# Performance work log

Measured on AMD Instinct MI355X. Metric: run time of the kernel, lower is better.

Reference implementation:

```python
import jax, jax.numpy as jnp
import numpy as np

N = 51200      # total nodes
G = 256        # graphs in batch
NPG = 200      # nodes per graph
E = 409600     # intra-graph edges
EPG = E // G
F_IN, HID, HEADS, NCLS = 768, 128, 4, 2


def setup_inputs() -> dict:
    key = jax.random.key(0)
    ks = jax.random.split(key, 20)
    x = jax.random.normal(ks[0], (N, F_IN), jnp.float32)
    # edges strictly inside each graph, no self-loops (PyG batching semantics)
    gid = jnp.arange(E, dtype=jnp.int32) // EPG
    sl = jax.random.randint(ks[1], (E,), 0, NPG, dtype=jnp.int32)
    off = jax.random.randint(ks[2], (E,), 1, NPG, dtype=jnp.int32)
    dl = (sl + off) % NPG
    edge_index = jnp.stack([gid * NPG + sl, gid * NPG + dl])
    batch = jnp.arange(N, dtype=jnp.int32) // NPG

    def glorot(k, shape, fan_in):
        return jax.random.normal(k, shape, jnp.float32) * np.float32(1.0 / np.sqrt(fan_in))

    return {
        'x': x, 'edge_index': edge_index, 'batch': batch,
        'W1': glorot(ks[3], (F_IN, HEADS * HID), F_IN),
        'a_src1': glorot(ks[4], (HEADS, HID), HID),
        'a_dst1': glorot(ks[5], (HEADS, HID), HID),
        'b1': jnp.zeros((HEADS * HID,), jnp.float32),
        'W2': glorot(ks[6], (HEADS * HID, HID), HEADS * HID),
        'a_src2': glorot(ks[7], (1, HID), HID),
        'a_dst2': glorot(ks[8], (1, HID), HID),
        'b2': jnp.zeros((HID,), jnp.float32),
        'Wc': glorot(ks[9], (HID, 2), HID),
        'bc': jnp.zeros((2,), jnp.float32),
        'Wf1': glorot(ks[10], (HID, HID), HID),
        'bf1': jnp.zeros((HID,), jnp.float32),
        'Wf2': glorot(ks[11], (HID, NCLS), HID),
        'bf2': jnp.zeros((NCLS,), jnp.float32),
    }


def _segment_softmax(logits, seg, num):
    m = jax.ops.segment_max(logits, seg, num_segments=num)
    e = jnp.exp(logits - m[seg])
    s = jax.ops.segment_sum(e, seg, num_segments=num)
    return e / (s[seg] + 1e-16)


def _gat(x, src, dst, W, a_s, a_d, b, n):
    # PyG GATConv, eval mode (attention dropout off), self-loops already in src/dst
    H, C = a_s.shape
    h = (x @ W).reshape(n, H, C)                       # [n,H,C]
    a_src = (h * a_s).sum(-1)                          # [n,H]
    a_dst = (h * a_d).sum(-1)
    logits = jax.nn.leaky_relu(a_src[src] + a_dst[dst], 0.2)  # [Etot,H]
    alpha = _segment_softmax(logits, dst, n)
    out = jax.ops.segment_sum(h[src] * alpha[:, :, None], dst, num_segments=n)
    return out.reshape(n, H * C) + b


def reference(x, edge_index, batch, W1, a_src1, a_dst1, b1, W2, a_src2, a_dst2, b2,
              Wc, bc, Wf1, bf1, Wf2, bf2):
    src0, dst0 = edge_index[0], edge_index[1]
    loop = jnp.arange(N, dtype=src0.dtype)
    src = jnp.concatenate([src0, loop])
    dst = jnp.concatenate([dst0, loop])

    h1 = jax.nn.relu(_gat(x, src, dst, W1, a_src1, a_dst1, b1, N))     # [N,512]
    h2 = jax.nn.relu(_gat(h1, src, dst, W2, a_src2, a_dst2, b2, N))    # [N,128]

    S = jax.nn.softmax(h2 @ Wc + bc, axis=1)                           # [N,2]

    # aggregate(): per-graph S^T A S via per-edge outer products (A from original edges)
    eg = batch[src0]
    outer = S[src0][:, :, None] * S[dst0][:, None, :]                  # [E,2,2]
    agg = jax.ops.segment_sum(outer, eg, num_segments=G)               # [G,2,2]
    rnorm = jnp.clip(jnp.abs(agg).sum(axis=2, keepdims=True), 1e-5, None)  # F.normalize p=1 dim=1
    nadj = agg / rnorm
    diag = jnp.diagonal(nadj, axis1=1, axis2=2)                        # [G,2]
    aggregate_loss = jnp.mean(jnp.mean((diag - 1.0) ** 2, axis=1))     # MSE vs ones, averaged over graphs

    # subgraph embedding: first row of S_g^T x_g per graph
    sub = jax.ops.segment_sum(S[:, 0:1] * h2, batch, num_segments=G)   # [G,128]

    out = jax.nn.relu(sub @ Wf1 + bf1)                                 # eval: dropout off
    out = out @ Wf2 + bf2                                              # [G,2]
    return out, aggregate_loss
```

## Files before the change

kernel.cpp:

```cpp
#include <hip/hip_runtime.h>
#include <hip/hip_bf16.h>
#include <cstdint>

#define N_NODES 51200
#define N_GRAPH 256
#define NPG     200
#define N_EDGE  409600
#define EPG     1600
#define F_IN    768
#define HID     128
#define HEADS   4
#define HC      512

typedef __attribute__((ext_vector_type(8))) short short8;
typedef __attribute__((ext_vector_type(4))) float floatx4;

constexpr size_t OFF_H1B    = 0;
constexpr size_t OFF_H2B    = OFF_H1B + (size_t)N_NODES * HC * 2;
constexpr size_t OFF_H2F    = OFF_H2B + (size_t)N_NODES * HID * 2;
constexpr size_t OFF_WT1    = OFF_H2F + (size_t)N_NODES * HID * 4;
constexpr size_t OFF_WT2    = OFF_WT1 + (size_t)HC * F_IN * 2;
constexpr size_t OFF_S      = OFF_WT2 + (size_t)HID * HC * 2;
constexpr size_t OFF_AGG    = OFF_S + (size_t)N_NODES * 2 * 4;
constexpr size_t OFF_SUB    = OFF_AGG + (size_t)N_GRAPH * 4 * 4;

__device__ __forceinline__ float leaky(float x) { return x >= 0.0f ? x : 0.2f * x; }

__device__ __forceinline__ unsigned short f2bf(float f) {
    unsigned int u = __float_as_uint(f);
    u += 0x7fffu + ((u >> 16) & 1u);
    return (unsigned short)(u >> 16);
}
__device__ __forceinline__ float bflo(int p) { return __uint_as_float((unsigned)p << 16); }
__device__ __forceinline__ float bfhi(int p) { return __uint_as_float((unsigned)p & 0xffff0000u); }

__device__ __forceinline__ void gl_lds16(const void* g, void* l) {
    __builtin_amdgcn_global_load_lds(
        (__attribute__((address_space(1))) void*)(g),
        (__attribute__((address_space(3))) void*)(l),
        16, 0, 0);
}

__global__ __launch_bounds__(256)
void transpose_cvt_kernel(const float* __restrict__ W, short* __restrict__ Wt,
                          int K, int Nn)
{
    int idx = blockIdx.x * 256 + threadIdx.x;
    if (idx >= K * Nn) return;
    int k = idx / Nn, n = idx % Nn;
    Wt[(size_t)n * K + k] = (short)f2bf(W[idx]);
}

template <bool A_BF16>
__global__ __launch_bounds__(256)
void gemm_mfma_kernel(const void* __restrict__ Av, const short* __restrict__ Bt,
                      unsigned short* __restrict__ C, int M, int Nn, int K)
{
    __shared__ __align__(16) short Ablob[4096];
    __shared__ __align__(16) short Bblob[4096];
    const int tid = threadIdx.x;
    const int w = tid >> 6, l = tid & 63;
    const int m0 = blockIdx.x * 128, n0 = blockIdx.y * 128;
    const int wr = w >> 1, wc = w & 1;

    floatx4 acc[4][4];
#pragma unroll
    for (int i = 0; i < 4; ++i)
#pragma unroll
        for (int j = 0; j < 4; ++j) acc[i][j] = (floatx4)0.0f;

    const short* bgp = Bt + (size_t)(n0 + (w * 2) * 16 + (l & 15)) * K + ((l >> 4) * 8);

    const float* Af = (const float*)Av;
    const short* Ab = (const short*)Av;
    const int r = tid >> 1, hh = tid & 1;
    const float* arow = Af + (size_t)(m0 + r) * K + hh * 16;
    const short* agp = Ab + (size_t)(m0 + (w * 2) * 16 + (l & 15)) * K + ((l >> 4) * 8);

    float4 pf0, pf1, pf2, pf3;
    if constexpr (!A_BF16) {
        pf0 = *(const float4*)(arow + 0);
        pf1 = *(const float4*)(arow + 4);
        pf2 = *(const float4*)(arow + 8);
        pf3 = *(const float4*)(arow + 12);
    }

    for (int k0 = 0; k0 < K; k0 += 32) {
        __syncthreads();
        if constexpr (A_BF16) {
            gl_lds16(agp + k0,          &Ablob[(w * 2) * 512]);
            gl_lds16(agp + 16 * K + k0, &Ablob[(w * 2 + 1) * 512]);
        } else {
            unsigned short us[16];
            us[0]=f2bf(pf0.x); us[1]=f2bf(pf0.y); us[2]=f2bf(pf0.z); us[3]=f2bf(pf0.w);
            us[4]=f2bf(pf1.x); us[5]=f2bf(pf1.y); us[6]=f2bf(pf1.z); us[7]=f2bf(pf1.w);
            us[8]=f2bf(pf2.x); us[9]=f2bf(pf2.y); us[10]=f2bf(pf2.z); us[11]=f2bf(pf2.w);
            us[12]=f2bf(pf3.x); us[13]=f2bf(pf3.y); us[14]=f2bf(pf3.z); us[15]=f2bf(pf3.w);
            const int o = (r >> 4) * 512 + (2 * hh) * 128 + (r & 15) * 8;
            short8 v0, v1;
#pragma unroll
            for (int j = 0; j < 8; ++j) { v0[j] = (short)us[j]; v1[j] = (short)us[8 + j]; }
            *(short8*)&Ablob[o]       = v0;
            *(short8*)&Ablob[o + 128] = v1;
        }
        gl_lds16(bgp + k0,          &Bblob[(w * 2) * 512]);
        gl_lds16(bgp + 16 * K + k0, &Bblob[(w * 2 + 1) * 512]);
        __syncthreads();

        if constexpr (!A_BF16) {
            if (k0 + 32 < K) {
                pf0 = *(const float4*)(arow + k0 + 32);
                pf1 = *(const float4*)(arow + k0 + 36);
                pf2 = *(const float4*)(arow + k0 + 40);
                pf3 = *(const float4*)(arow + k0 + 44);
            }
        }

        short8 af[4], bfr[4];
#pragma unroll
        for (int mi = 0; mi < 4; ++mi)
            af[mi] = *(const short8*)&Ablob[(wr * 4 + mi) * 512 + l * 8];
#pragma unroll
        for (int ni = 0; ni < 4; ++ni)
            bfr[ni] = *(const short8*)&Bblob[(wc * 4 + ni) * 512 + l * 8];
#pragma unroll
        for (int mi = 0; mi < 4; ++mi)
#pragma unroll
            for (int ni = 0; ni < 4; ++ni)
                acc[mi][ni] = __builtin_amdgcn_mfma_f32_16x16x32_bf16(
                    af[mi], bfr[ni], acc[mi][ni], 0, 0, 0);
    }

    const int lr = (l >> 4) * 4, lc = l & 15;
#pragma unroll
    for (int mi = 0; mi < 4; ++mi)
#pragma unroll
        for (int ni = 0; ni < 4; ++ni) {
            const size_t base = (size_t)(m0 + wr * 64 + mi * 16 + lr) * Nn
                              + (n0 + wc * 64 + ni * 16 + lc);
#pragma unroll
            for (int rr = 0; rr < 4; ++rr)
                C[base + (size_t)rr * Nn] = f2bf(acc[mi][ni][rr]);
        }
}

__global__ __launch_bounds__(512)
void gat1_kernel(const unsigned short* __restrict__ H, const int* __restrict__ src0,
                 const int* __restrict__ dst0, const float* __restrict__ a_s,
                 const float* __restrict__ a_d, const float* __restrict__ b1,
                 unsigned short* __restrict__ out)
{
    const int g = blockIdx.x, h = blockIdx.y;
    __shared__ int   s_feat[NPG * 64];
    __shared__ float s_as[NPG], s_ad[NPG], s_m[NPG], s_inv[NPG];
    __shared__ int   s_row[NPG + 1];
    __shared__ int   s_cnt[NPG];
    __shared__ int   s_scan[256];
    __shared__ unsigned short s_eraw[EPG];
    __shared__ int2  s_wc[EPG];
    const int tid = threadIdx.x, w = tid >> 6, l = tid & 63;
    const int gbase = g * NPG;

    for (int flat = tid; flat < NPG * 16; flat += 512) {
        int row = flat >> 4, q = flat & 15;
        uint4 v = *(const uint4*)(H + (size_t)(gbase + row) * HC + h * HID + q * 8);
        *(uint4*)&s_feat[row * 64 + q * 4] = v;
    }
    for (int j = tid; j < EPG; j += 512) {
        int s = src0[g * EPG + j] - gbase;
        int d = dst0[g * EPG + j] - gbase;
        s_eraw[j] = (unsigned short)(s | (d << 8));
    }
    if (tid < NPG) s_cnt[tid] = 0;
    __syncthreads();

    for (int j = tid; j < EPG; j += 512)
        atomicAdd(&s_cnt[s_eraw[j] >> 8], 1);
    const float2 av = ((const float2*)(a_s + h * HID))[l];
    const float2 dv = ((const float2*)(a_d + h * HID))[l];
    for (int nl = w; nl < NPG; nl += 8) {
        int pk = s_feat[nl * 64 + l];
        float f0 = bflo(pk), f1 = bfhi(pk);
        float ss = f0 * av.x + f1 * av.y;
        float sd = f0 * dv.x + f1 * dv.y;
#pragma unroll
        for (int off = 1; off < 64; off <<= 1) {
            ss += __shfl_xor(ss, off);
            sd += __shfl_xor(sd, off);
        }
        if (l == 0) { s_as[nl] = ss; s_ad[nl] = sd; }
    }
    __syncthreads();

    {
        int v = (tid < NPG) ? s_cnt[tid] : 0;
        if (tid < 256) s_scan[tid] = v;
        __syncthreads();
        for (int off = 1; off < 256; off <<= 1) {
            int u = (tid >= off && tid < 256) ? s_scan[tid - off] : 0;
            __syncthreads();
            if (tid < 256) s_scan[tid] += u;
            __syncthreads();
        }
        if (tid < NPG) s_row[tid + 1] = s_scan[tid];
        if (tid == 0) s_row[0] = 0;
        __syncthreads();
        if (tid < NPG) s_scan[tid] = s_row[tid];
    }
    __syncthreads();

    for (int j = tid; j < EPG; j += 512) {
        int pk = s_eraw[j];
        int p = atomicAdd(&s_scan[pk >> 8], 1);
        s_wc[p].y = pk;
    }
    __syncthreads();

    for (int j = tid; j < EPG; j += 512) {
        int pk = s_wc[j].y;
        s_wc[j].x = __float_as_int(leaky(s_as[pk & 255] + s_ad[pk >> 8]));
    }
    __syncthreads();

    if (tid < NPG) {
        float m = leaky(s_as[tid] + s_ad[tid]);
        int r0 = s_row[tid], r1 = s_row[tid + 1];
        for (int j = r0; j < r1; ++j) m = fmaxf(m, __int_as_float(s_wc[j].x));
        s_m[tid] = m;
    }
    __syncthreads();

    for (int j = tid; j < EPG; j += 512) {
        int2 e = s_wc[j];
        s_wc[j].x = __float_as_int(__expf(__int_as_float(e.x) - s_m[e.y >> 8]));
    }
    __syncthreads();

    if (tid < NPG) {
        float rs = __expf(leaky(s_as[tid] + s_ad[tid]) - s_m[tid]);
        int r0 = s_row[tid], r1 = s_row[tid + 1];
        for (int j = r0; j < r1; ++j) rs += __int_as_float(s_wc[j].x);
        s_inv[tid] = 1.0f / (rs + 1e-16f);
    }
    __syncthreads();

    const float2 bv = ((const float2*)(b1 + h * HID))[l];
    for (int nl = w; nl < NPG; nl += 8) {
        const int r0 = s_row[nl], r1 = s_row[nl + 1];
        const float wself = __expf(leaky(s_as[nl] + s_ad[nl]) - s_m[nl]);
        int spk = s_feat[nl * 64 + l];
        float a0 = wself * bflo(spk), a1 = wself * bfhi(spk);
        float c0 = 0.0f, c1 = 0.0f;
        int j = r0;
        for (; j + 4 <= r1; j += 4) {
            int2 e0 = s_wc[j], e1 = s_wc[j + 1], e2 = s_wc[j + 2], e3 = s_wc[j + 3];
            int p0 = s_feat[(e0.y & 255) * 64 + l];
            int p1 = s_feat[(e1.y & 255) * 64 + l];
            int p2 = s_feat[(e2.y & 255) * 64 + l];
            int p3 = s_feat[(e3.y & 255) * 64 + l];
            float w0 = __int_as_float(e0.x), w1 = __int_as_float(e1.x);
            float w2 = __int_as_float(e2.x), w3 = __int_as_float(e3.x);
            a0 += w0 * bflo(p0); a1 += w0 * bfhi(p0);
            c0 += w1 * bflo(p1); c1 += w1 * bfhi(p1);
            a0 += w2 * bflo(p2); a1 += w2 * bfhi(p2);
            c0 += w3 * bflo(p3); c1 += w3 * bfhi(p3);
        }
        for (; j < r1; ++j) {
            int2 e0 = s_wc[j];
            int p0 = s_feat[(e0.y & 255) * 64 + l];
            float w0 = __int_as_float(e0.x);
            a0 += w0 * bflo(p0); a1 += w0 * bfhi(p0);
        }
        const float inv = s_inv[nl];
        float o0 = (a0 + c0) * inv + bv.x;
        float o1 = (a1 + c1) * inv + bv.y;
        unsigned int st = (unsigned int)f2bf(fmaxf(o0, 0.0f))
                        | ((unsigned int)f2bf(fmaxf(o1, 0.0f)) << 16);
        *(unsigned int*)&out[(size_t)(gbase + nl) * HC + h * HID + 2 * l] = st;
    }
}

__global__ __launch_bounds__(512)
void gat2_kernel(const unsigned short* __restrict__ H, const int* __restrict__ src0,
                 const int* __restrict__ dst0, const float* __restrict__ a_s,
                 const float* __restrict__ a_d, const float* __restrict__ b2,
                 const float* __restrict__ Wc, const float* __restrict__ bc,
                 float* __restrict__ h2, float* __restrict__ S)
{
    const int g = blockIdx.x;
    __shared__ int   s_feat[NPG * 64];
    __shared__ float s_as[NPG], s_ad[NPG], s_m[NPG], s_inv[NPG];
    __shared__ int   s_row[NPG + 1];
    __shared__ int   s_cnt[NPG];
    __shared__ int   s_scan[256];
    __shared__ unsigned short s_eraw[EPG];
    __shared__ int2  s_wc[EPG];
    const int tid = threadIdx.x, w = tid >> 6, l = tid & 63;
    const int gbase = g * NPG;

    for (int flat = tid; flat < NPG * 16; flat += 512) {
        int row = flat >> 4, q = flat & 15;
        uint4 v = *(const uint4*)(H + (size_t)(gbase + row) * HID + q * 8);
        *(uint4*)&s_feat[row * 64 + q * 4] = v;
    }
    for (int j = tid; j < EPG; j += 512) {
        int s = src0[g * EPG + j] - gbase;
        int d = dst0[g * EPG + j] - gbase;
        s_eraw[j] = (unsigned short)(s | (d << 8));
    }
    if (tid < NPG) s_cnt[tid] = 0;
    __syncthreads();

    for (int j = tid; j < EPG; j += 512)
        atomicAdd(&s_cnt[s_eraw[j] >> 8], 1);
    const float2 av = ((const float2*)a_s)[l];
    const float2 dv = ((const float2*)a_d)[l];
    for (int nl = w; nl < NPG; nl += 8) {
        int pk = s_feat[nl * 64 + l];
        float f0 = bflo(pk), f1 = bfhi(pk);
        float ss = f0 * av.x + f1 * av.y;
        float sd = f0 * dv.x + f1 * dv.y;
#pragma unroll
        for (int off = 1; off < 64; off <<= 1) {
            ss += __shfl_xor(ss, off);
            sd += __shfl_xor(sd, off);
        }
        if (l == 0) { s_as[nl] = ss; s_ad[nl] = sd; }
    }
    __syncthreads();

    {
        int v = (tid < NPG) ? s_cnt[tid] : 0;
        if (tid < 256) s_scan[tid] = v;
        __syncthreads();
        for (int off = 1; off < 256; off <<= 1) {
            int u = (tid >= off && tid < 256) ? s_scan[tid - off] : 0;
            __syncthreads();
            if (tid < 256) s_scan[tid] += u;
            __syncthreads();
        }
        if (tid < NPG) s_row[tid + 1] = s_scan[tid];
        if (tid == 0) s_row[0] = 0;
        __syncthreads();
        if (tid < NPG) s_scan[tid] = s_row[tid];
    }
    __syncthreads();

    for (int j = tid; j < EPG; j += 512) {
        int pk = s_eraw[j];
        int p = atomicAdd(&s_scan[pk >> 8], 1);
        s_wc[p].y = pk;
    }
    __syncthreads();

    for (int j = tid; j < EPG; j += 512) {
        int pk = s_wc[j].y;
        s_wc[j].x = __float_as_int(leaky(s_as[pk & 255] + s_ad[pk >> 8]));
    }
    __syncthreads();

    if (tid < NPG) {
        float m = leaky(s_as[tid] + s_ad[tid]);
        int r0 = s_row[tid], r1 = s_row[tid + 1];
        for (int j = r0; j < r1; ++j) m = fmaxf(m, __int_as_float(s_wc[j].x));
        s_m[tid] = m;
    }
    __syncthreads();

    for (int j = tid; j < EPG; j += 512) {
        int2 e = s_wc[j];
        s_wc[j].x = __float_as_int(__expf(__int_as_float(e.x) - s_m[e.y >> 8]));
    }
    __syncthreads();

    if (tid < NPG) {
        float rs = __expf(leaky(s_as[tid] + s_ad[tid]) - s_m[tid]);
        int r0 = s_row[tid], r1 = s_row[tid + 1];
        for (int j = r0; j < r1; ++j) rs += __int_as_float(s_wc[j].x);
        s_inv[tid] = 1.0f / (rs + 1e-16f);
    }
    __syncthreads();

    const float2 bv = ((const float2*)b2)[l];
    const float4 wcv = ((const float4*)Wc)[l];
    const float bc0 = bc[0], bc1 = bc[1];
    for (int nl = w; nl < NPG; nl += 8) {
        const int r0 = s_row[nl], r1 = s_row[nl + 1];
        const float wself = __expf(leaky(s_as[nl] + s_ad[nl]) - s_m[nl]);
        int spk = s_feat[nl * 64 + l];
        float a0 = wself * bflo(spk), a1 = wself * bfhi(spk);
        float c0 = 0.0f, c1 = 0.0f;
        int j = r0;
        for (; j + 4 <= r1; j += 4) {
            int2 e0 = s_wc[j], e1 = s_wc[j + 1], e2 = s_wc[j + 2], e3 = s_wc[j + 3];
            int p0 = s_feat[(e0.y & 255) * 64 + l];
            int p1 = s_feat[(e1.y & 255) * 64 + l];
            int p2 = s_feat[(e2.y & 255) * 64 + l];
            int p3 = s_feat[(e3.y & 255) * 64 + l];
            float w0 = __int_as_float(e0.x), w1 = __int_as_float(e1.x);
            float w2 = __int_as_float(e2.x), w3 = __int_as_float(e3.x);
            a0 += w0 * bflo(p0); a1 += w0 * bfhi(p0);
            c0 += w1 * bflo(p1); c1 += w1 * bfhi(p1);
            a0 += w2 * bflo(p2); a1 += w2 * bfhi(p2);
            c0 += w3 * bflo(p3); c1 += w3 * bfhi(p3);
        }
        for (; j < r1; ++j) {
            int2 e0 = s_wc[j];
            int p0 = s_feat[(e0.y & 255) * 64 + l];
            float w0 = __int_as_float(e0.x);
            a0 += w0 * bflo(p0); a1 += w0 * bfhi(p0);
        }
        const float inv = s_inv[nl];
        float o0 = fmaxf((a0 + c0) * inv + bv.x, 0.0f);
        float o1 = fmaxf((a1 + c1) * inv + bv.y, 0.0f);
        *(float2*)&h2[(size_t)(gbase + nl) * HID + 2 * l] = make_float2(o0, o1);
        float z0 = o0 * wcv.x + o1 * wcv.z;
        float z1 = o0 * wcv.y + o1 * wcv.w;
#pragma unroll
        for (int off = 1; off < 64; off <<= 1) {
            z0 += __shfl_xor(z0, off);
            z1 += __shfl_xor(z1, off);
        }
        if (l == 0) {
            z0 += bc0; z1 += bc1;
            float mm = fmaxf(z0, z1);
            float e0 = __expf(z0 - mm), e1 = __expf(z1 - mm);
            float is = 1.0f / (e0 + e1);
            *(float2*)&S[(size_t)(gbase + nl) * 2] = make_float2(e0 * is, e1 * is);
        }
    }
}

__global__ __launch_bounds__(256)
void agg_kernel(const int* __restrict__ src0, const int* __restrict__ dst0,
                const float* __restrict__ S, float* __restrict__ agg)
{
    const int g = blockIdx.x, tid = threadIdx.x;
    float a00 = 0, a01 = 0, a10 = 0, a11 = 0;
    for (int e = g*EPG + tid; e < (g + 1)*EPG; e += 256) {
        int s = src0[e], d = dst0[e];
        float s0 = S[s*2], s1 = S[s*2 + 1];
        float d0 = S[d*2], d1 = S[d*2 + 1];
        a00 += s0*d0; a01 += s0*d1; a10 += s1*d0; a11 += s1*d1;
    }
    for (int off = 32; off > 0; off >>= 1) {
        a00 += __shfl_down(a00, off); a01 += __shfl_down(a01, off);
        a10 += __shfl_down(a10, off); a11 += __shfl_down(a11, off);
    }
    __shared__ float sred[4][4];
    if ((tid & 63) == 0) {
        int w = tid >> 6;
        sred[w][0] = a00; sred[w][1] = a01; sred[w][2] = a10; sred[w][3] = a11;
    }
    __syncthreads();
    if (tid == 0) {
        agg[g*4 + 0] = sred[0][0] + sred[1][0] + sred[2][0] + sred[3][0];
        agg[g*4 + 1] = sred[0][1] + sred[1][1] + sred[2][1] + sred[3][1];
        agg[g*4 + 2] = sred[0][2] + sred[1][2] + sred[2][2] + sred[3][2];
        agg[g*4 + 3] = sred[0][3] + sred[1][3] + sred[2][3] + sred[3][3];
    }
}

__global__ __launch_bounds__(256)
void loss_kernel(const float* __restrict__ agg, float* __restrict__ out_loss)
{
    int tid = threadIdx.x;
    float a00 = agg[tid*4 + 0], a01 = agg[tid*4 + 1];
    float a10 = agg[tid*4 + 2], a11 = agg[tid*4 + 3];
    float rn0 = fmaxf(fabsf(a00) + fabsf(a01), 1e-5f);
    float rn1 = fmaxf(fabsf(a10) + fabsf(a11), 1e-5f);
    float d0 = a00 / rn0 - 1.0f, d1 = a11 / rn1 - 1.0f;
    float contrib = 0.5f * (d0*d0 + d1*d1);
    for (int off = 32; off > 0; off >>= 1) contrib += __shfl_down(contrib, off);
    __shared__ float sred[4];
    if ((tid & 63) == 0) sred[tid >> 6] = contrib;
    __syncthreads();
    if (tid == 0)
        out_loss[0] = (sred[0] + sred[1] + sred[2] + sred[3]) * (1.0f / N_GRAPH);
}

__global__ __launch_bounds__(128)
void sub_kernel(const float* __restrict__ S, const float* __restrict__ h2,
                float* __restrict__ sub)
{
    const int g = blockIdx.x, c = threadIdx.x;
    const float* Sg = S + (size_t)g * NPG * 2;
    const float* hg = h2 + (size_t)g * NPG * HID;
    float acc = 0.0f;
    for (int i = 0; i < NPG; ++i)
        acc += Sg[i*2] * hg[(size_t)i*HID + c];
    sub[g*HID + c] = acc;
}

__global__ __launch_bounds__(128)
void final_kernel(const float* __restrict__ sub, const float* __restrict__ Wf1,
                  const float* __restrict__ bf1, const float* __restrict__ Wf2,
                  const float* __restrict__ bf2, float* __restrict__ out)
{
    __shared__ float s_sub[128];
    __shared__ float s_fc[128];
    const int g = blockIdx.x, t = threadIdx.x;
    s_sub[t] = sub[g*HID + t];
    __syncthreads();
    float acc = bf1[t];
    for (int c = 0; c < 128; ++c)
        acc += s_sub[c] * Wf1[c*128 + t];
    s_fc[t] = fmaxf(acc, 0.0f);
    __syncthreads();
    if (t < 2) {
        float z = bf2[t];
        for (int j = 0; j < 128; ++j) z += s_fc[j] * Wf2[j*2 + t];
        out[g*2 + t] = z;
    }
}

extern "C" void kernel_launch(void* const* d_in, const int* in_sizes, int n_in,
                              void* d_out, int out_size, void* d_ws, size_t ws_size,
                              hipStream_t stream)
{
    const float* x   = (const float*)d_in[0];
    const int*   ei  = (const int*)d_in[1];
    const float* W1  = (const float*)d_in[3];
    const float* as1 = (const float*)d_in[4];
    const float* ad1 = (const float*)d_in[5];
    const float* b1  = (const float*)d_in[6];
    const float* W2  = (const float*)d_in[7];
    const float* as2 = (const float*)d_in[8];
    const float* ad2 = (const float*)d_in[9];
    const float* b2  = (const float*)d_in[10];
    const float* Wc  = (const float*)d_in[11];
    const float* bc  = (const float*)d_in[12];
    const float* Wf1 = (const float*)d_in[13];
    const float* bf1 = (const float*)d_in[14];
    const float* Wf2 = (const float*)d_in[15];
    const float* bf2 = (const float*)d_in[16];
    const int* src0 = ei;
    const int* dst0 = ei + N_EDGE;

    char* ws = (char*)d_ws;
    unsigned short* H1b = (unsigned short*)(ws + OFF_H1B);
    unsigned short* H2b = (unsigned short*)(ws + OFF_H2B);
    float* h2    = (float*)(ws + OFF_H2F);
    short* Wt1   = (short*)(ws + OFF_WT1);
    short* Wt2   = (short*)(ws + OFF_WT2);
    float* Sbuf  = (float*)(ws + OFF_S);
    float* aggb  = (float*)(ws + OFF_AGG);
    float* subb  = (float*)(ws + OFF_SUB);
    float* out   = (float*)d_out;

    transpose_cvt_kernel<<<(F_IN*HC + 255)/256, 256, 0, stream>>>(W1, Wt1, F_IN, HC);
    transpose_cvt_kernel<<<(HC*HID + 255)/256, 256, 0, stream>>>(W2, Wt2, HC, HID);

    gemm_mfma_kernel<false><<<dim3(N_NODES/128, HC/128), 256, 0, stream>>>(
        x, Wt1, H1b, N_NODES, HC, F_IN);

    gat1_kernel<<<dim3(N_GRAPH, HEADS), 512, 0, stream>>>(
        H1b, src0, dst0, as1, ad1, b1, H1b);

    gemm_mfma_kernel<true><<<dim3(N_NODES/128, HID/128), 256, 0, stream>>>(
        H1b, Wt2, H2b, N_NODES, HID, HC);

    gat2_kernel<<<N_GRAPH, 512, 0, stream>>>(
        H2b, src0, dst0, as2, ad2, b2, Wc, bc, h2, Sbuf);

    agg_kernel<<<N_GRAPH, 256, 0, stream>>>(src0, dst0, Sbuf, aggb);
    loss_kernel<<<1, 256, 0, stream>>>(aggb, out + N_GRAPH*2);

    sub_kernel<<<N_GRAPH, 128, 0, stream>>>(Sbuf, h2, subb);
    final_kernel<<<N_GRAPH, 128, 0, stream>>>(subb, Wf1, bf1, Wf2, bf2, out);

    (void)in_sizes; (void)n_in; (void)out_size; (void)ws_size;
}
```

Baseline: 520.1 us.

## Replace LDS-staged GEMM with register-direct MFMA operand loads and double buffering

The GEMM kernel no longer stages A and B tiles through shared memory with barriers. Each wave loads its MFMA fragments directly from global memory into registers, converting fp32 A to bf16 in registers when needed. A two-stage register double buffer over 64-wide K steps overlaps the next loads with the current MFMAs. This removes LDS traffic and __syncthreads. The cost is duplicated global/L2 reads across waves, which share no data through LDS, and higher register pressure.

```diff
diff --git a/kernel.cpp b/kernel.cpp
--- a/kernel.cpp
+++ b/kernel.cpp
@@ -34,11 +34,13 @@
 __device__ __forceinline__ float bflo(int p) { return __uint_as_float((unsigned)p << 16); }
 __device__ __forceinline__ float bfhi(int p) { return __uint_as_float((unsigned)p & 0xffff0000u); }
 
-__device__ __forceinline__ void gl_lds16(const void* g, void* l) {
-    __builtin_amdgcn_global_load_lds(
-        (__attribute__((address_space(1))) void*)(g),
-        (__attribute__((address_space(3))) void*)(l),
-        16, 0, 0);
+__device__ __forceinline__ short8 cvt8(float4 lo, float4 hi) {
+    short8 r;
+    r[0] = (short)f2bf(lo.x); r[1] = (short)f2bf(lo.y);
+    r[2] = (short)f2bf(lo.z); r[3] = (short)f2bf(lo.w);
+    r[4] = (short)f2bf(hi.x); r[5] = (short)f2bf(hi.y);
+    r[6] = (short)f2bf(hi.z); r[7] = (short)f2bf(hi.w);
+    return r;
 }
 
 __global__ __launch_bounds__(256)
@@ -53,15 +55,14 @@
 
 template <bool A_BF16>
 __global__ __launch_bounds__(256)
-void gemm_mfma_kernel(const void* __restrict__ Av, const short* __restrict__ Bt,
-                      unsigned short* __restrict__ C, int M, int Nn, int K)
-{
-    __shared__ __align__(16) short Ablob[4096];
-    __shared__ __align__(16) short Bblob[4096];
+void gemm_reg_kernel(const void* __restrict__ Av, const short* __restrict__ Bt,
+                     unsigned short* __restrict__ C, int M, int Nn, int K)
+{
     const int tid = threadIdx.x;
     const int w = tid >> 6, l = tid & 63;
     const int m0 = blockIdx.x * 128, n0 = blockIdx.y * 128;
     const int wr = w >> 1, wc = w & 1;
+    const int row = l & 15, quad = l >> 4;
 
     floatx4 acc[4][4];
 #pragma unroll
@@ -69,69 +70,94 @@
 #pragma unroll
         for (int j = 0; j < 4; ++j) acc[i][j] = (floatx4)0.0f;
 
-    const short* bgp = Bt + (size_t)(n0 + (w * 2) * 16 + (l & 15)) * K + ((l >> 4) * 8);
-
-    const float* Af = (const float*)Av;
-    const short* Ab = (const short*)Av;
-    const int r = tid >> 1, hh = tid & 1;
-    const float* arow = Af + (size_t)(m0 + r) * K + hh * 16;
-    const short* agp = Ab + (size_t)(m0 + (w * 2) * 16 + (l & 15)) * K + ((l >> 4) * 8);
-
-    float4 pf0, pf1, pf2, pf3;
+    const float* ap32[4];
+    const short* ap16[4];
+    const short* bp[4];
+#pragma unroll
+    for (int i = 0; i < 4; ++i) {
+        const size_t aoff = (size_t)(m0 + wr * 64 + i * 16 + row) * K + quad * 8;
+        ap32[i] = (const float*)Av + aoff;
+        ap16[i] = (const short*)Av + aoff;
+        bp[i]   = Bt + (size_t)(n0 + wc * 64 + i * 16 + row) * K + quad * 8;
+    }
+
+    short8 aA[4], aB[4], bA[4], bB[4];
+    float4 rAlo[4], rAhi[4], rBlo[4], rBhi[4];
+
+    if constexpr (A_BF16) {
+#pragma unroll
+        for (int i = 0; i < 4; ++i) aA[i] = *(const short8*)(ap16[i]);
+    } else {
+#pragma unroll
+        for (int i = 0; i < 4; ++i) {
+            rAlo[i] = *(const float4*)(ap32[i]);
+            rAhi[i] = *(const float4*)(ap32[i] + 4);
+        }
+    }
+#pragma unroll
+    for (int i = 0; i < 4; ++i) bA[i] = *(const short8*)(bp[i]);
     if constexpr (!A_BF16) {
-        pf0 = *(const float4*)(arow + 0);
-        pf1 = *(const float4*)(arow + 4);
-        pf2 = *(const float4*)(arow + 8);
-        pf3 = *(const float4*)(arow + 12);
-    }
-
-    for (int k0 = 0; k0 < K; k0 += 32) {
-        __syncthreads();
+#pragma unroll
+        for (int i = 0; i < 4; ++i) aA[i] = cvt8(rAlo[i], rAhi[i]);
+    }
+
+    for (int k0 = 0; k0 < K; k0 += 64) {
         if constexpr (A_BF16) {
-            gl_lds16(agp + k0,          &Ablob[(w * 2) * 512]);
-            gl_lds16(agp + 16 * K + k0, &Ablob[(w * 2 + 1) * 512]);
+#pragma unroll
+            for (int i = 0; i < 4; ++i) aB[i] = *(const short8*)(ap16[i] + k0 + 32);
         } else {
-            unsigned short us[16];
-            us[0]=f2bf(pf0.x); us[1]=f2bf(pf0.y); us[2]=f2bf(pf0.z); us[3]=f2bf(pf0.w);
-            us[4]=f2bf(pf1.x); us[5]=f2bf(pf1.y); us[6]=f2bf(pf1.z); us[7]=f2bf(pf1.w);
-            us[8]=f2bf(pf2.x); us[9]=f2bf(pf2.y); us[10]=f2bf(pf2.z); us[11]=f2bf(pf2.w);
-            us[12]=f2bf(pf3.x); us[13]=f2bf(pf3.y); us[14]=f2bf(pf3.z); us[15]=f2bf(pf3.w);
-            const int o = (r >> 4) * 512 + (2 * hh) * 128 + (r & 15) * 8;
-            short8 v0, v1;
-#pragma unroll
-            for (int j = 0; j < 8; ++j) { v0[j] = (short)us[j]; v1[j] = (short)us[8 + j]; }
-            *(short8*)&Ablob[o]       = v0;
-            *(short8*)&Ablob[o + 128] = v1;
-        }
-        gl_lds16(bgp + k0,          &Bblob[(w * 2) * 512]);
-        gl_lds16(bgp + 16 * K + k0, &Bblob[(w * 2 + 1) * 512]);
-        __syncthreads();
-
-        if constexpr (!A_BF16) {
-            if (k0 + 32 < K) {
-                pf0 = *(const float4*)(arow + k0 + 32);
-                pf1 = *(const float4*)(arow + k0 + 36);
-                pf2 = *(const float4*)(arow + k0 + 40);
-                pf3 = *(const float4*)(arow + k0 + 44);
+#pragma unroll
+            for (int i = 0; i < 4; ++i) {
+                rBlo[i] = *(const float4*)(ap32[i] + k0 + 32);
+                rBhi[i] = *(const float4*)(ap32[i] + k0 + 36);
             }
         }
-
-        short8 af[4], bfr[4];
-#pragma unroll
-        for (int mi = 0; mi < 4; ++mi)
-            af[mi] = *(const short8*)&Ablob[(wr * 4 + mi) * 512 + l * 8];
-#pragma unroll
-        for (int ni = 0; ni < 4; ++ni)
-            bfr[ni] = *(const short8*)&Bblob[(wc * 4 + ni) * 512 + l * 8];
+#pragma unroll
+        for (int i = 0; i < 4; ++i) bB[i] = *(const short8*)(bp[i] + k0 + 32);
+
 #pragma unroll
         for (int mi = 0; mi < 4; ++mi)
 #pragma unroll
             for (int ni = 0; ni < 4; ++ni)
                 acc[mi][ni] = __builtin_amdgcn_mfma_f32_16x16x32_bf16(
-                    af[mi], bfr[ni], acc[mi][ni], 0, 0, 0);
-    }
-
-    const int lr = (l >> 4) * 4, lc = l & 15;
+                    aA[mi], bA[ni], acc[mi][ni], 0, 0, 0);
+
+        if constexpr (!A_BF16) {
+#pragma unroll
+            for (int i = 0; i < 4; ++i) aB[i] = cvt8(rBlo[i], rBhi[i]);
+        }
+
+        if (k0 + 64 < K) {
+            if constexpr (A_BF16) {
+#pragma unroll
+                for (int i = 0; i < 4; ++i) aA[i] = *(const short8*)(ap16[i] + k0 + 64);
+            } else {
+#pragma unroll
+                for (int i = 0; i < 4; ++i) {
+                    rAlo[i] = *(const float4*)(ap32[i] + k0 + 64);
+                    rAhi[i] = *(const float4*)(ap32[i] + k0 + 68);
+                }
+            }
+#pragma unroll
+            for (int i = 0; i < 4; ++i) bA[i] = *(const short8*)(bp[i] + k0 + 64);
+        }
+
+#pragma unroll
+        for (int mi = 0; mi < 4; ++mi)
+#pragma unroll
+            for (int ni = 0; ni < 4; ++ni)
+                acc[mi][ni] = __builtin_amdgcn_mfma_f32_16x16x32_bf16(
+                    aB[mi], bB[ni], acc[mi][ni], 0, 0, 0);
+
+        if constexpr (!A_BF16) {
+            if (k0 + 64 < K) {
+#pragma unroll
+                for (int i = 0; i < 4; ++i) aA[i] = cvt8(rAlo[i], rAhi[i]);
+            }
+        }
+    }
+
+    const int lr = quad * 4, lc = row;
 #pragma unroll
     for (int mi = 0; mi < 4; ++mi)
 #pragma unroll
@@ -551,13 +577,13 @@
     transpose_cvt_kernel<<<(F_IN*HC + 255)/256, 256, 0, stream>>>(W1, Wt1, F_IN, HC);
     transpose_cvt_kernel<<<(HC*HID + 255)/256, 256, 0, stream>>>(W2, Wt2, HC, HID);
 
-    gemm_mfma_kernel<false><<<dim3(N_NODES/128, HC/128), 256, 0, stream>>>(
+    gemm_reg_kernel<false><<<dim3(N_NODES/128, HC/128), 256, 0, stream>>>(
         x, Wt1, H1b, N_NODES, HC, F_IN);
 
     gat1_kernel<<<dim3(N_GRAPH, HEADS), 512, 0, stream>>>(
         H1b, src0, dst0, as1, ad1, b1, H1b);
 
-    gemm_mfma_kernel<true><<<dim3(N_NODES/128, HID/128), 256, 0, stream>>>(
+    gemm_reg_kernel<true><<<dim3(N_NODES/128, HID/128), 256, 0, stream>>>(
         H1b, Wt2, H2b, N_NODES, HID, HC);
 
     gat2_kernel<<<N_GRAPH, 512, 0, stream>>>(
```

Measured after the change: 636.2 us. +22.3%, slower.

## Pre-convert x to bf16 and deepen GEMM K-tile with direct LDS loads

Applied to the files above, without the earlier changes.

Adds a separate kernel that converts the fp32 input x to bf16 once, so the first GEMM can use the same global-to-LDS direct-load path as the second GEMM instead of converting in registers. The unified GEMM kernel now processes a K-step of 64 per iteration (two MFMA k-groups per barrier pair) with doubled LDS tiles and a launch-bounds occupancy hint. This trades an extra full read and write of x (about 150MB of fp32 read plus bf16 write) for fewer barriers and better load issue in the GEMMs.

```diff
diff --git a/kernel.cpp b/kernel.cpp
--- a/kernel.cpp
+++ b/kernel.cpp
@@ -23,6 +23,7 @@
 constexpr size_t OFF_S      = OFF_WT2 + (size_t)HID * HC * 2;
 constexpr size_t OFF_AGG    = OFF_S + (size_t)N_NODES * 2 * 4;
 constexpr size_t OFF_SUB    = OFF_AGG + (size_t)N_GRAPH * 4 * 4;
+constexpr size_t OFF_XB     = OFF_SUB + (size_t)N_GRAPH * HID * 4;
 
 __device__ __forceinline__ float leaky(float x) { return x >= 0.0f ? x : 0.2f * x; }
 
@@ -33,6 +34,15 @@
 }
 __device__ __forceinline__ float bflo(int p) { return __uint_as_float((unsigned)p << 16); }
 __device__ __forceinline__ float bfhi(int p) { return __uint_as_float((unsigned)p & 0xffff0000u); }
+
+__device__ __forceinline__ short8 cvt8(float4 lo, float4 hi) {
+    short8 r;
+    r[0] = (short)f2bf(lo.x); r[1] = (short)f2bf(lo.y);
+    r[2] = (short)f2bf(lo.z); r[3] = (short)f2bf(lo.w);
+    r[4] = (short)f2bf(hi.x); r[5] = (short)f2bf(hi.y);
+    r[6] = (short)f2bf(hi.z); r[7] = (short)f2bf(hi.w);
+    return r;
+}
 
 __device__ __forceinline__ void gl_lds16(const void* g, void* l) {
     __builtin_amdgcn_global_load_lds(
@@ -42,6 +52,15 @@
 }
 
 __global__ __launch_bounds__(256)
+void cvt_x_kernel(const float* __restrict__ X, short* __restrict__ Xb)
+{
+    int i = blockIdx.x * 256 + threadIdx.x;
+    float4 lo = ((const float4*)X)[i * 2];
+    float4 hi = ((const float4*)X)[i * 2 + 1];
+    *(short8*)&Xb[(size_t)i * 8] = cvt8(lo, hi);
+}
+
+__global__ __launch_bounds__(256)
 void transpose_cvt_kernel(const float* __restrict__ W, short* __restrict__ Wt,
                           int K, int Nn)
 {
@@ -51,17 +70,17 @@
     Wt[(size_t)n * K + k] = (short)f2bf(W[idx]);
 }
 
-template <bool A_BF16>
-__global__ __launch_bounds__(256)
-void gemm_mfma_kernel(const void* __restrict__ Av, const short* __restrict__ Bt,
+__global__ __launch_bounds__(256, 3)
+void gemm_bf16_kernel(const short* __restrict__ A, const short* __restrict__ Bt,
                       unsigned short* __restrict__ C, int M, int Nn, int K)
 {
-    __shared__ __align__(16) short Ablob[4096];
-    __shared__ __align__(16) short Bblob[4096];
+    __shared__ __align__(16) short Ablob[8192];
+    __shared__ __align__(16) short Bblob[8192];
     const int tid = threadIdx.x;
     const int w = tid >> 6, l = tid & 63;
     const int m0 = blockIdx.x * 128, n0 = blockIdx.y * 128;
     const int wr = w >> 1, wc = w & 1;
+    const int row = l & 15, quad = l >> 4;
 
     floatx4 acc[4][4];
 #pragma unroll
@@ -69,69 +88,42 @@
 #pragma unroll
         for (int j = 0; j < 4; ++j) acc[i][j] = (floatx4)0.0f;
 
-    const short* bgp = Bt + (size_t)(n0 + (w * 2) * 16 + (l & 15)) * K + ((l >> 4) * 8);
-
-    const float* Af = (const float*)Av;
-    const short* Ab = (const short*)Av;
-    const int r = tid >> 1, hh = tid & 1;
-    const float* arow = Af + (size_t)(m0 + r) * K + hh * 16;
-    const short* agp = Ab + (size_t)(m0 + (w * 2) * 16 + (l & 15)) * K + ((l >> 4) * 8);
-
-    float4 pf0, pf1, pf2, pf3;
-    if constexpr (!A_BF16) {
-        pf0 = *(const float4*)(arow + 0);
-        pf1 = *(const float4*)(arow + 4);
-        pf2 = *(const float4*)(arow + 8);
-        pf3 = *(const float4*)(arow + 12);
-    }
-
-    for (int k0 = 0; k0 < K; k0 += 32) {
+    const short* agp[4];
+    const short* bgp[4];
+#pragma unroll
+    for (int i = 0; i < 4; ++i) {
+        int a = w * 4 + i;
+        agp[i] = A  + (size_t)(m0 + (a >> 1) * 16 + row) * K + (a & 1) * 32 + quad * 8;
+        bgp[i] = Bt + (size_t)(n0 + (a >> 1) * 16 + row) * K + (a & 1) * 32 + quad * 8;
+    }
+
+    for (int k0 = 0; k0 < K; k0 += 64) {
         __syncthreads();
-        if constexpr (A_BF16) {
-            gl_lds16(agp + k0,          &Ablob[(w * 2) * 512]);
-            gl_lds16(agp + 16 * K + k0, &Ablob[(w * 2 + 1) * 512]);
-        } else {
-            unsigned short us[16];
-            us[0]=f2bf(pf0.x); us[1]=f2bf(pf0.y); us[2]=f2bf(pf0.z); us[3]=f2bf(pf0.w);
-            us[4]=f2bf(pf1.x); us[5]=f2bf(pf1.y); us[6]=f2bf(pf1.z); us[7]=f2bf(pf1.w);
-            us[8]=f2bf(pf2.x); us[9]=f2bf(pf2.y); us[10]=f2bf(pf2.z); us[11]=f2bf(pf2.w);
-            us[12]=f2bf(pf3.x); us[13]=f2bf(pf3.y); us[14]=f2bf(pf3.z); us[15]=f2bf(pf3.w);
-            const int o = (r >> 4) * 512 + (2 * hh) * 128 + (r & 15) * 8;
-            short8 v0, v1;
-#pragma unroll
-            for (int j = 0; j < 8; ++j) { v0[j] = (short)us[j]; v1[j] = (short)us[8 + j]; }
-            *(short8*)&Ablob[o]       = v0;
-            *(short8*)&Ablob[o + 128] = v1;
-        }
-        gl_lds16(bgp + k0,          &Bblob[(w * 2) * 512]);
-        gl_lds16(bgp + 16 * K + k0, &Bblob[(w * 2 + 1) * 512]);
+#pragma unroll
+        for (int i = 0; i < 4; ++i) {
+            gl_lds16(agp[i] + k0, &Ablob[(w * 4 + i) * 512]);
+            gl_lds16(bgp[i] + k0, &Bblob[(w * 4 + i) * 512]);
+        }
         __syncthreads();
-
-        if constexpr (!A_BF16) {
-            if (k0 + 32 < K) {
-                pf0 = *(const float4*)(arow + k0 + 32);
-                pf1 = *(const float4*)(arow + k0 + 36);
-                pf2 = *(const float4*)(arow + k0 + 40);
-                pf3 = *(const float4*)(arow + k0 + 44);
-            }
-        }
-
-        short8 af[4], bfr[4];
-#pragma unroll
-        for (int mi = 0; mi < 4; ++mi)
-            af[mi] = *(const short8*)&Ablob[(wr * 4 + mi) * 512 + l * 8];
-#pragma unroll
-        for (int ni = 0; ni < 4; ++ni)
-            bfr[ni] = *(const short8*)&Bblob[(wc * 4 + ni) * 512 + l * 8];
-#pragma unroll
-        for (int mi = 0; mi < 4; ++mi)
+#pragma unroll
+        for (int kg = 0; kg < 2; ++kg) {
+            short8 af[4], bfr[4];
+#pragma unroll
+            for (int mi = 0; mi < 4; ++mi)
+                af[mi] = *(const short8*)&Ablob[((wr * 4 + mi) * 2 + kg) * 512 + l * 8];
 #pragma unroll
             for (int ni = 0; ni < 4; ++ni)
-                acc[mi][ni] = __builtin_amdgcn_mfma_f32_16x16x32_bf16(
-                    af[mi], bfr[ni], acc[mi][ni], 0, 0, 0);
-    }
-
-    const int lr = (l >> 4) * 4, lc = l & 15;
+                bfr[ni] = *(const short8*)&Bblob[((wc * 4 + ni) * 2 + kg) * 512 + l * 8];
+#pragma unroll
+            for (int mi = 0; mi < 4; ++mi)
+#pragma unroll
+                for (int ni = 0; ni < 4; ++ni)
+                    acc[mi][ni] = __builtin_amdgcn_mfma_f32_16x16x32_bf16(
+                        af[mi], bfr[ni], acc[mi][ni], 0, 0, 0);
+        }
+    }
+
+    const int lr = quad * 4, lc = row;
 #pragma unroll
     for (int mi = 0; mi < 4; ++mi)
 #pragma unroll
@@ -543,22 +535,24 @@
     float* h2    = (float*)(ws + OFF_H2F);
     short* Wt1   = (short*)(ws + OFF_WT1);
     short* Wt2   = (short*)(ws + OFF_WT2);
+    short* Xb    = (short*)(ws + OFF_XB);
     float* Sbuf  = (float*)(ws + OFF_S);
     float* aggb  = (float*)(ws + OFF_AGG);
     float* subb  = (float*)(ws + OFF_SUB);
     float* out   = (float*)d_out;
 
+    cvt_x_kernel<<<(N_NODES * F_IN / 8) / 256, 256, 0, stream>>>(x, Xb);
     transpose_cvt_kernel<<<(F_IN*HC + 255)/256, 256, 0, stream>>>(W1, Wt1, F_IN, HC);
     transpose_cvt_kernel<<<(HC*HID + 255)/256, 256, 0, stream>>>(W2, Wt2, HC, HID);
 
-    gemm_mfma_kernel<false><<<dim3(N_NODES/128, HC/128), 256, 0, stream>>>(
-        x, Wt1, H1b, N_NODES, HC, F_IN);
+    gemm_bf16_kernel<<<dim3(N_NODES/128, HC/128), 256, 0, stream>>>(
+        Xb, Wt1, H1b, N_NODES, HC, F_IN);
 
     gat1_kernel<<<dim3(N_GRAPH, HEADS), 512, 0, stream>>>(
         H1b, src0, dst0, as1, ad1, b1, H1b);
 
-    gemm_mfma_kernel<true><<<dim3(N_NODES/128, HID/128), 256, 0, stream>>>(
-        H1b, Wt2, H2b, N_NODES, HID, HC);
+    gemm_bf16_kernel<<<dim3(N_NODES/128, HID/128), 256, 0, stream>>>(
+        (const short*)H1b, Wt2, H2b, N_NODES, HID, HC);
 
     gat2_kernel<<<N_GRAPH, 512, 0, stream>>>(
         H2b, src0, dst0, as2, ad2, b2, Wc, bc, h2, Sbuf);
```

New measurement: 521.5 us. Within noise of the previous version (+0.3%).
